# Performance work log

Measured on AMD Instinct MI355X. Metric: run time of the kernel, lower is better.

The kernel has to match this reference:

```python
import jax, jax.numpy as jnp
import numpy as np

N = 100000        # nodes
E = 1600000       # edges
G = 1000          # graphs
DIM = 256         # dim_h
DEPTH = 4
VOCAB = 100
MAX_ND = 20
EPS = 1e-5


def setup_inputs() -> dict:
    key = jax.random.key(0)
    ks = jax.random.split(key, 24)
    inp = {
        "x_idx": jax.random.randint(ks[0], (N,), 0, VOCAB, dtype=jnp.int32),
        "node_depth": jax.random.randint(ks[1], (N,), 0, MAX_ND, dtype=jnp.int32),
        "edge_index": jax.random.randint(ks[2], (2, E), 0, N, dtype=jnp.int32),
        "batch": jnp.sort(jax.random.randint(ks[3], (N,), 0, G, dtype=jnp.int32)),
        # node encoder embeddings
        "emb_node": 0.02 * jax.random.normal(ks[4], (VOCAB, DIM), jnp.float32),
        "emb_depth": 0.02 * jax.random.normal(ks[5], (MAX_ND, DIM), jnp.float32),
        # per-depth GIN MLP: Linear(DIM,DIM) -> ReLU -> Linear(DIM,DIM)
        "gin_w1": 0.05 * jax.random.normal(ks[6], (DEPTH, DIM, DIM), jnp.float32),
        "gin_b1": jnp.zeros((DEPTH, DIM), jnp.float32),
        "gin_w2": 0.05 * jax.random.normal(ks[7], (DEPTH, DIM, DIM), jnp.float32),
        "gin_b2": jnp.zeros((DEPTH, DIM), jnp.float32),
        # GraphNorm params
        "gn_alpha": jnp.ones((DEPTH, DIM), jnp.float32),
        "gn_gamma": jnp.ones((DEPTH, DIM), jnp.float32),
        "gn_beta": jnp.zeros((DEPTH, DIM), jnp.float32),
        # attention gate MLP: Linear(DIM, 2*DIM) -> ReLU -> Linear(2*DIM, 1)
        "att_w1": 0.05 * jax.random.normal(ks[8], (DEPTH, DIM, 2 * DIM), jnp.float32),
        "att_b1": jnp.zeros((DEPTH, 2 * DIM), jnp.float32),
        "att_w2": 0.05 * jax.random.normal(ks[9], (DEPTH, 2 * DIM, 1), jnp.float32),
        "att_b2": jnp.zeros((DEPTH, 1), jnp.float32),
    }
    return inp


def _graph_norm(x, batch, alpha, gamma, beta):
    # per-graph GraphNorm (Cai et al.): shift by alpha*mean, scale by std
    cnt = jax.ops.segment_sum(jnp.ones((x.shape[0],), x.dtype), batch, num_segments=G)
    cnt = jnp.maximum(cnt, 1.0)[:, None]                     # [G,1]
    mean = jax.ops.segment_sum(x, batch, num_segments=G) / cnt
    out = x - alpha * mean[batch]
    var = jax.ops.segment_sum(out * out, batch, num_segments=G) / cnt
    inv = jax.lax.rsqrt(var + EPS)
    return gamma * out * inv[batch] + beta


def _att_pool(x, batch, w1, b1, w2, b2):
    gate = (jax.nn.relu(x @ w1 + b1) @ w2 + b2)[:, 0]        # [N]
    m = jax.ops.segment_max(gate, batch, num_segments=G)
    e = jnp.exp(gate - m[batch])
    denom = jax.ops.segment_sum(e, batch, num_segments=G)
    w = e / denom[batch]                                     # segment softmax
    return jax.ops.segment_sum(w[:, None] * x, batch, num_segments=G)  # [G,DIM]


def reference(x_idx, node_depth, edge_index, batch,
              emb_node, emb_depth,
              gin_w1, gin_b1, gin_w2, gin_b2,
              gn_alpha, gn_gamma, gn_beta,
              att_w1, att_b1, att_w2, att_b2):
    src, dst = edge_index[0], edge_index[1]
    x = emb_node[x_idx] + emb_depth[node_depth]              # node encoder [N,DIM]
    graph_embs = []
    for d in range(DEPTH):
        x_in = x
        # GINConv (eps=0): MLP(x + sum_{j->i} x_j)
        agg = jax.ops.segment_sum(x[src], dst, num_segments=N)
        h = x + agg
        x = jax.nn.relu(h @ gin_w1[d] + gin_b1[d]) @ gin_w2[d] + gin_b2[d]
        x = _graph_norm(x, batch, gn_alpha[d], gn_gamma[d], gn_beta[d])
        if d < DEPTH - 1:
            x = jax.nn.relu(x)
        x = x + x_in                                         # residual
        graph_embs.append(_att_pool(x, batch, att_w1[d], att_b1[d], att_w2[d], att_b2[d]))
    stacked = jnp.stack(graph_embs, axis=0)                  # [DEPTH,G,DIM]
    agg_emb = jnp.mean(stacked, axis=0)                      # MLAP-Mean aggregate
    return jnp.concatenate([stacked, agg_emb[None]], axis=0) # [DEPTH+1,G,DIM]
```

## Files before the change

### kernel.cpp

```cpp
#include <hip/hip_runtime.h>
#include <hip/hip_bf16.h>

#define NN 100000
#define EE 1600000
#define GG 1000
#define DIMH 256
#define NDEPTH 4
static constexpr float EPSV = 1e-5f;

typedef unsigned short ushort;
typedef __attribute__((ext_vector_type(8))) ushort ushort8v;
typedef __attribute__((ext_vector_type(8))) short short8v;
typedef __attribute__((ext_vector_type(4))) float f32x4;

__device__ __forceinline__ float bf2f(ushort u) {
    return __uint_as_float(((unsigned)u) << 16);
}
__device__ __forceinline__ ushort f2bf(float f) {
    unsigned u = __float_as_uint(f);
    unsigned r = u + 0x7FFFu + ((u >> 16) & 1u);
    return (ushort)(r >> 16);
}

__global__ __launch_bounds__(256) void k_graph_bounds(const int* __restrict__ batch, int* __restrict__ gstart) {
    int g = blockIdx.x * 256 + threadIdx.x;
    if (g > GG) return;
    int lo = 0, hi = NN;
    while (lo < hi) { int mid = (lo + hi) >> 1; if (batch[mid] < g) lo = mid + 1; else hi = mid; }
    gstart[g] = lo;
}

__global__ __launch_bounds__(256) void k_hist(const int* __restrict__ dst, int* __restrict__ deg) {
    int e = blockIdx.x * 256 + threadIdx.x;
    if (e < EE) atomicAdd(&deg[dst[e]], 1);
}

__global__ __launch_bounds__(256) void k_scan_a(const int* __restrict__ deg, int* __restrict__ rs, int* __restrict__ part) {
    __shared__ int s[256];
    int t = threadIdx.x;
    int i = blockIdx.x * 256 + t;
    int v = (i < NN) ? deg[i] : 0;
    s[t] = v; __syncthreads();
    for (int off = 1; off < 256; off <<= 1) {
        int u = (t >= off) ? s[t - off] : 0;
        __syncthreads();
        s[t] += u;
        __syncthreads();
    }
    if (i < NN) rs[i] = s[t] - v;
    if (t == 255) part[blockIdx.x] = s[255];
}

__global__ __launch_bounds__(512) void k_scan_b(int* __restrict__ part, int nb, int* __restrict__ rs) {
    __shared__ int s[512];
    int t = threadIdx.x;
    int v = (t < nb) ? part[t] : 0;
    s[t] = v; __syncthreads();
    for (int off = 1; off < 512; off <<= 1) {
        int u = (t >= off) ? s[t - off] : 0;
        __syncthreads();
        s[t] += u;
        __syncthreads();
    }
    if (t < nb) part[t] = s[t] - v;
    if (t == 0) rs[NN] = EE;
}

__global__ __launch_bounds__(256) void k_scan_c(int* __restrict__ rs, const int* __restrict__ part) {
    int i = blockIdx.x * 256 + threadIdx.x;
    if (i < NN) rs[i] += part[blockIdx.x];
}

__global__ __launch_bounds__(256) void k_copy_int(const int* __restrict__ a, int* __restrict__ b, int n) {
    int i = blockIdx.x * 256 + threadIdx.x;
    if (i < n) b[i] = a[i];
}

__global__ __launch_bounds__(256) void k_scatter(const int* __restrict__ src, const int* __restrict__ dst,
                                                 int* __restrict__ cursor, int* __restrict__ col) {
    int e = blockIdx.x * 256 + threadIdx.x;
    if (e >= EE) return;
    int d = dst[e];
    int pos = atomicAdd(&cursor[d], 1);
    col[pos] = src[e];
}

__global__ __launch_bounds__(256) void k_wtrans(const float* __restrict__ in, ushort* __restrict__ out_hi,
                                                ushort* __restrict__ out_lo, int K, int N) {
    int d = blockIdx.z;
    in  += (size_t)d * K * N;
    out_hi += (size_t)d * K * N;
    out_lo += (size_t)d * K * N;
    int n0 = blockIdx.x * 32, k0 = blockIdx.y * 32;
    int t = threadIdx.x;
    int tx = t & 31, ty = t >> 5;
    __shared__ float tile[32][33];
#pragma unroll
    for (int j = 0; j < 4; j++) tile[ty + 8 * j][tx] = in[(size_t)(k0 + ty + 8 * j) * N + n0 + tx];
    __syncthreads();
#pragma unroll
    for (int j = 0; j < 4; j++) {
        float f = tile[tx][ty + 8 * j];
        ushort hi = f2bf(f);
        float lo = f - bf2f(hi);
        size_t o = (size_t)(n0 + ty + 8 * j) * K + k0 + tx;
        out_hi[o] = hi;
        out_lo[o] = f2bf(lo);
    }
}

__global__ __launch_bounds__(256) void k_encoder(const int* __restrict__ xidx, const int* __restrict__ ndep,
                                                 const float* __restrict__ en, const float* __restrict__ ed,
                                                 ushort* __restrict__ x) {
    int gi = blockIdx.x * 256 + threadIdx.x;
    int node = gi >> 6, q = gi & 63;
    if (node >= NN) return;
    float4 va = ((const float4*)en)[(size_t)xidx[node] * 64 + q];
    float4 vb = ((const float4*)ed)[(size_t)ndep[node] * 64 + q];
    ushort4 o;
    o.x = f2bf(va.x + vb.x); o.y = f2bf(va.y + vb.y);
    o.z = f2bf(va.z + vb.z); o.w = f2bf(va.w + vb.w);
    ((ushort4*)x)[gi] = o;
}

__global__ __launch_bounds__(256) void k_aggregate(const ushort* __restrict__ x, const int* __restrict__ rs,
                                                   const int* __restrict__ col, ushort* __restrict__ hb) {
    int node = blockIdx.x * 4 + (threadIdx.x >> 6);
    int lane = threadIdx.x & 63;
    if (node >= NN) return;
    const ushort4* x4 = (const ushort4*)x;
    ushort4 sv = x4[(size_t)node * 64 + lane];
    float a0 = bf2f(sv.x), a1 = bf2f(sv.y), a2 = bf2f(sv.z), a3 = bf2f(sv.w);
    float b0 = 0.f, b1 = 0.f, b2 = 0.f, b3 = 0.f;
    float c0 = 0.f, c1 = 0.f, c2 = 0.f, c3 = 0.f;
    float d0 = 0.f, d1 = 0.f, d2 = 0.f, d3 = 0.f;
    int s = rs[node], e = rs[node + 1];
    int j = s;
    for (; j + 4 <= e; j += 4) {
        int i0 = col[j], i1 = col[j + 1], i2 = col[j + 2], i3 = col[j + 3];
        ushort4 v0 = x4[(size_t)i0 * 64 + lane];
        ushort4 v1 = x4[(size_t)i1 * 64 + lane];
        ushort4 v2 = x4[(size_t)i2 * 64 + lane];
        ushort4 v3 = x4[(size_t)i3 * 64 + lane];
        a0 += bf2f(v0.x); a1 += bf2f(v0.y); a2 += bf2f(v0.z); a3 += bf2f(v0.w);
        b0 += bf2f(v1.x); b1 += bf2f(v1.y); b2 += bf2f(v1.z); b3 += bf2f(v1.w);
        c0 += bf2f(v2.x); c1 += bf2f(v2.y); c2 += bf2f(v2.z); c3 += bf2f(v2.w);
        d0 += bf2f(v3.x); d1 += bf2f(v3.y); d2 += bf2f(v3.z); d3 += bf2f(v3.w);
    }
    for (; j < e; j++) {
        int c = col[j];
        ushort4 v = x4[(size_t)c * 64 + lane];
        a0 += bf2f(v.x); a1 += bf2f(v.y); a2 += bf2f(v.z); a3 += bf2f(v.w);
    }
    a0 += b0 + c0 + d0; a1 += b1 + c1 + d1; a2 += b2 + c2 + d2; a3 += b3 + c3 + d3;
    ushort4 o; o.x = f2bf(a0); o.y = f2bf(a1); o.z = f2bf(a2); o.w = f2bf(a3);
    ((ushort4*)hb)[(size_t)node * 64 + lane] = o;
}

template<int MODE>
__global__ __launch_bounds__(256, 2) void k_mfma_gemm(const ushort* __restrict__ A,
                                                      const ushort* __restrict__ Bhi,
                                                      const ushort* __restrict__ Blo,
                                                      const float* __restrict__ bias,
                                                      const float* __restrict__ w2,
                                                      ushort* __restrict__ C,
                                                      float* __restrict__ partial,
                                                      int M) {
    __shared__ __align__(16) ushort As[256 * 64];
    __shared__ __align__(16) ushort Bh[128 * 64];
    __shared__ __align__(16) ushort Bl[128 * 64];
    int t = threadIdx.x;
    int wv = t >> 6, l = t & 63;
    int wr = wv >> 1, wc = wv & 1;
    int row0 = blockIdx.x * 256;
    int col0 = blockIdx.y * 128;

    f32x4 acc[8][4];
#pragma unroll
    for (int m = 0; m < 8; m++)
#pragma unroll
        for (int n = 0; n < 4; n++) acc[m][n] = (f32x4){0.f, 0.f, 0.f, 0.f};

    int srow_in = l >> 3;
    int slot    = l & 7;

    for (int k0 = 0; k0 < 256; k0 += 64) {
#pragma unroll
        for (int i = 0; i < 8; i++) {
            int stripe = wv * 8 + i;
            int rl = stripe * 8 + srow_in;
            int gc = slot ^ (rl & 7);
            const ushort* ga = A + (size_t)min(row0 + rl, M - 1) * 256 + k0 + gc * 8;
            __builtin_amdgcn_global_load_lds((const __attribute__((address_space(1))) void*)ga,
                                             (__attribute__((address_space(3))) void*)(As + stripe * 512),
                                             16, 0, 0);
        }
#pragma unroll
        for (int i = 0; i < 4; i++) {
            int stripe = wv * 4 + i;
            int rl = stripe * 8 + srow_in;
            int gc = slot ^ (rl & 7);
            const ushort* gh = Bhi + (size_t)(col0 + rl) * 256 + k0 + gc * 8;
            __builtin_amdgcn_global_load_lds((const __attribute__((address_space(1))) void*)gh,
                                             (__attribute__((address_space(3))) void*)(Bh + stripe * 512),
                                             16, 0, 0);
            const ushort* gl = Blo + (size_t)(col0 + rl) * 256 + k0 + gc * 8;
            __builtin_amdgcn_global_load_lds((const __attribute__((address_space(1))) void*)gl,
                                             (__attribute__((address_space(3))) void*)(Bl + stripe * 512),
                                             16, 0, 0);
        }
        __syncthreads();
#pragma unroll
        for (int s = 0; s < 2; s++) {
            short8v af[8], bhf[4], blf[4];
#pragma unroll
            for (int m = 0; m < 8; m++) {
                int rl = wr * 128 + m * 16 + (l & 15);
                int ch = (s * 4 + (l >> 4)) ^ (rl & 7);
                af[m] = *(const short8v*)(As + rl * 64 + ch * 8);
            }
#pragma unroll
            for (int n = 0; n < 4; n++) {
                int rl = wc * 64 + n * 16 + (l & 15);
                int ch = (s * 4 + (l >> 4)) ^ (rl & 7);
                bhf[n] = *(const short8v*)(Bh + rl * 64 + ch * 8);
                blf[n] = *(const short8v*)(Bl + rl * 64 + ch * 8);
            }
#pragma unroll
            for (int m = 0; m < 8; m++)
#pragma unroll
                for (int n = 0; n < 4; n++) {
                    acc[m][n] = __builtin_amdgcn_mfma_f32_16x16x32_bf16(af[m], bhf[n], acc[m][n], 0, 0, 0);
                    acc[m][n] = __builtin_amdgcn_mfma_f32_16x16x32_bf16(af[m], blf[n], acc[m][n], 0, 0, 0);
                }
        }
        __syncthreads();
    }

    if (MODE == 2) {
        float b1v[4], w2v[4];
#pragma unroll
        for (int n = 0; n < 4; n++) {
            int colc = col0 + wc * 64 + n * 16 + (l & 15);
            b1v[n] = bias[colc];
            w2v[n] = w2[colc];
        }
#pragma unroll
        for (int m = 0; m < 8; m++) {
#pragma unroll
            for (int j = 0; j < 4; j++) {
                float p = 0.f;
#pragma unroll
                for (int n = 0; n < 4; n++) {
                    float v = fmaxf(acc[m][n][j] + b1v[n], 0.f);
                    p = fmaf(v, w2v[n], p);
                }
#pragma unroll
                for (int off = 1; off < 16; off <<= 1) p += __shfl_xor(p, off, 64);
                if ((l & 15) == 0) {
                    int row = row0 + wr * 128 + m * 16 + ((l >> 4) << 2) + j;
                    if (row < M) partial[(size_t)row * 8 + blockIdx.y * 2 + wc] = p;
                }
            }
        }
    } else {
        float bv[4];
#pragma unroll
        for (int n = 0; n < 4; n++) bv[n] = bias[col0 + wc * 64 + n * 16 + (l & 15)];
#pragma unroll
        for (int m = 0; m < 8; m++) {
#pragma unroll
            for (int j = 0; j < 4; j++) {
                int row = row0 + wr * 128 + m * 16 + ((l >> 4) << 2) + j;
                if (row < M) {
#pragma unroll
                    for (int n = 0; n < 4; n++) {
                        float v = acc[m][n][j] + bv[n];
                        if (MODE == 1) v = fmaxf(v, 0.f);
                        C[(size_t)row * 256 + col0 + wc * 64 + n * 16 + (l & 15)] = f2bf(v);
                    }
                }
            }
        }
    }
}

__global__ __launch_bounds__(256) void k_gatefin(const float* __restrict__ partial, const float* __restrict__ b2,
                                                 float* __restrict__ gate) {
    int i = blockIdx.x * 256 + threadIdx.x;
    if (i >= NN) return;
    const float4* p = (const float4*)(partial + (size_t)i * 8);
    float4 u = p[0], v = p[1];
    gate[i] = u.x + u.y + u.z + u.w + v.x + v.y + v.z + v.w + b2[0];
}

__global__ __launch_bounds__(256) void k_stats(const ushort* __restrict__ y, const int* __restrict__ gstart,
                                               const float* __restrict__ alpha,
                                               float* __restrict__ mean, float* __restrict__ inv) {
    int g = blockIdx.x, t = threadIdx.x;
    int s = gstart[g], e = gstart[g + 1];
    float s1 = 0.f, s2 = 0.f;
    for (int i = s; i < e; i++) {
        float v = bf2f(y[(size_t)i * DIMH + t]);
        s1 += v; s2 = fmaf(v, v, s2);
    }
    float cnt = (float)((e - s) > 1 ? (e - s) : 1);
    float m = s1 / cnt;
    float a = alpha[t];
    float am = a * m;
    float var = s2 / cnt - 2.f * am * m + am * am;
    mean[(size_t)g * DIMH + t] = m;
    inv[(size_t)g * DIMH + t] = rsqrtf(var + EPSV);
}

__global__ __launch_bounds__(256) void k_norm(const ushort* __restrict__ y, const int* __restrict__ batch,
                                              const float* __restrict__ mean, const float* __restrict__ inv,
                                              const float* __restrict__ alpha, const float* __restrict__ gamma,
                                              const float* __restrict__ beta, ushort* __restrict__ x, int relu) {
    int gi = blockIdx.x * 256 + threadIdx.x;
    int node = gi >> 6, q = gi & 63;
    if (node >= NN) return;
    int b = batch[node];
    ushort4 yv = ((const ushort4*)y)[gi];
    ushort4 xv = ((const ushort4*)x)[gi];
    float vv[4] = { bf2f(yv.x), bf2f(yv.y), bf2f(yv.z), bf2f(yv.w) };
    float xo[4] = { bf2f(xv.x), bf2f(xv.y), bf2f(xv.z), bf2f(xv.w) };
#pragma unroll
    for (int c = 0; c < 4; c++) {
        int colc = q * 4 + c;
        float m  = mean[(size_t)b * DIMH + colc];
        float iv = inv[(size_t)b * DIMH + colc];
        float o = (vv[c] - alpha[colc] * m) * iv * gamma[colc] + beta[colc];
        if (relu) o = fmaxf(o, 0.f);
        xo[c] += o;
    }
    ushort4 o4; o4.x = f2bf(xo[0]); o4.y = f2bf(xo[1]); o4.z = f2bf(xo[2]); o4.w = f2bf(xo[3]);
    ((ushort4*)x)[gi] = o4;
}

__global__ __launch_bounds__(256) void k_pool(const ushort* __restrict__ x, const float* __restrict__ gate,
                                              const int* __restrict__ gstart, float* __restrict__ outg) {
    __shared__ float red[256];
    __shared__ float wbuf[256];
    int g = blockIdx.x, t = threadIdx.x;
    int s = gstart[g], e = gstart[g + 1];
    if (s >= e) { outg[(size_t)g * DIMH + t] = 0.f; return; }
    float m = -3.4e38f;
    for (int i = s + t; i < e; i += 256) m = fmaxf(m, gate[i]);
    red[t] = m; __syncthreads();
    for (int o = 128; o > 0; o >>= 1) { if (t < o) red[t] = fmaxf(red[t], red[t + o]); __syncthreads(); }
    m = red[0]; __syncthreads();
    float se = 0.f;
    for (int i = s + t; i < e; i += 256) se += expf(gate[i] - m);
    red[t] = se; __syncthreads();
    for (int o = 128; o > 0; o >>= 1) { if (t < o) red[t] += red[t + o]; __syncthreads(); }
    float inv_se = 1.f / red[0];
    float o_acc = 0.f;
    for (int base = s; base < e; base += 256) {
        __syncthreads();
        int i = base + t;
        wbuf[t] = (i < e) ? expf(gate[i] - m) * inv_se : 0.f;
        __syncthreads();
        int cnt = min(256, e - base);
        for (int j = 0; j < cnt; j++) o_acc += wbuf[j] * bf2f(x[(size_t)(base + j) * DIMH + t]);
    }
    outg[(size_t)g * DIMH + t] = o_acc;
}

__global__ __launch_bounds__(256) void k_final(float* __restrict__ out) {
    const int GD = GG * DIMH;
    int i = blockIdx.x * 256 + threadIdx.x;
    if (i >= GD) return;
    float s = out[i] + out[GD + i] + out[2 * GD + i] + out[3 * GD + i];
    out[4 * GD + i] = 0.25f * s;
}

__global__ __launch_bounds__(256) void k_zero_out(float* __restrict__ out, int n) {
    int i = blockIdx.x * 256 + threadIdx.x;
    if (i < n) out[i] = 0.f;
}

extern "C" void kernel_launch(void* const* d_in, const int* in_sizes, int n_in,
                              void* d_out, int out_size, void* d_ws, size_t ws_size,
                              hipStream_t stream) {
    const int*   x_idx     = (const int*)d_in[0];
    const int*   node_dep  = (const int*)d_in[1];
    const int*   eidx      = (const int*)d_in[2];
    const int*   batch     = (const int*)d_in[3];
    const float* emb_node  = (const float*)d_in[4];
    const float* emb_depth = (const float*)d_in[5];
    const float* gin_w1    = (const float*)d_in[6];
    const float* gin_b1    = (const float*)d_in[7];
    const float* gin_w2    = (const float*)d_in[8];
    const float* gin_b2    = (const float*)d_in[9];
    const float* gn_alpha  = (const float*)d_in[10];
    const float* gn_gamma  = (const float*)d_in[11];
    const float* gn_beta   = (const float*)d_in[12];
    const float* att_w1    = (const float*)d_in[13];
    const float* att_b1    = (const float*)d_in[14];
    const float* att_w2    = (const float*)d_in[15];
    const float* att_b2    = (const float*)d_in[16];
    float* out = (float*)d_out;
    (void)in_sizes; (void)n_in;

    const size_t SZ_NODE_BF16 = (size_t)NN * DIMH * 2;
    const size_t SZ_W256 = (size_t)NDEPTH * 256 * 256 * 2;
    const size_t SZ_W512 = (size_t)NDEPTH * 256 * 512 * 2;
    size_t required = 3 * ((SZ_NODE_BF16 + 255) & ~(size_t)255)
                    + 4 * SZ_W256 + 2 * SZ_W512
                    + ((size_t)EE * 4 + 256) + ((size_t)(NN + 1) * 4 + 256) * 2
                    + 4096 + 8192 + 2 * ((size_t)GG * DIMH * 4 + 256) + ((size_t)NN * 4 + 256) + 65536;
    if (ws_size < required) {
        k_zero_out<<<(out_size + 255) / 256, 256, 0, stream>>>(out, out_size);
        return;
    }

    char* w = (char*)d_ws;
    size_t off = 0;
    auto alloc = [&](size_t bytes) -> char* {
        char* p = w + off;
        off += (bytes + 255) & ~(size_t)255;
        return p;
    };
    ushort* x  = (ushort*)alloc(SZ_NODE_BF16);
    ushort* hb = (ushort*)alloc(SZ_NODE_BF16);
    ushort* y1 = (ushort*)alloc(SZ_NODE_BF16);
    float* partial = (float*)y1;
    ushort* wt_g1h = (ushort*)alloc(SZ_W256);
    ushort* wt_g1l = (ushort*)alloc(SZ_W256);
    ushort* wt_g2h = (ushort*)alloc(SZ_W256);
    ushort* wt_g2l = (ushort*)alloc(SZ_W256);
    ushort* wt_a1h = (ushort*)alloc(SZ_W512);
    ushort* wt_a1l = (ushort*)alloc(SZ_W512);
    int* deg    = (int*)alloc((size_t)NN * 4);
    int* rs     = (int*)alloc((size_t)(NN + 1) * 4);
    int* part   = (int*)alloc(512 * 4);
    int* gstart = (int*)alloc((GG + 1) * 4);
    int* col    = (int*)alloc((size_t)EE * 4);
    float* mean = (float*)alloc((size_t)GG * DIMH * 4);
    float* inv  = (float*)alloc((size_t)GG * DIMH * 4);
    float* gate = (float*)alloc((size_t)NN * 4);

    const int* src  = eidx;
    const int* dstp = eidx + EE;

    hipMemsetAsync(deg, 0, (size_t)NN * 4, stream);
    k_graph_bounds<<<(GG + 1 + 255) / 256, 256, 0, stream>>>(batch, gstart);
    k_hist<<<(EE + 255) / 256, 256, 0, stream>>>(dstp, deg);
    int nb = (NN + 255) / 256;
    k_scan_a<<<nb, 256, 0, stream>>>(deg, rs, part);
    k_scan_b<<<1, 512, 0, stream>>>(part, nb, rs);
    k_scan_c<<<nb, 256, 0, stream>>>(rs, part);
    k_copy_int<<<nb, 256, 0, stream>>>(rs, deg, NN);
    k_scatter<<<(EE + 255) / 256, 256, 0, stream>>>(src, dstp, deg, col);
    k_encoder<<<(NN * 64 + 255) / 256, 256, 0, stream>>>(x_idx, node_dep, emb_node, emb_depth, x);

    k_wtrans<<<dim3(8, 8, NDEPTH), 256, 0, stream>>>(gin_w1, wt_g1h, wt_g1l, 256, 256);
    k_wtrans<<<dim3(8, 8, NDEPTH), 256, 0, stream>>>(gin_w2, wt_g2h, wt_g2l, 256, 256);
    k_wtrans<<<dim3(16, 8, NDEPTH), 256, 0, stream>>>(att_w1, wt_a1h, wt_a1l, 256, 512);

    const int GD = GG * DIMH;
    const int MB = (NN + 255) / 256;
    for (int d = 0; d < NDEPTH; d++) {
        k_aggregate<<<(NN + 3) / 4, 256, 0, stream>>>(x, rs, col, hb);
        k_mfma_gemm<1><<<dim3(MB, 2), 256, 0, stream>>>(hb, wt_g1h + (size_t)d * 65536, wt_g1l + (size_t)d * 65536,
                                                        gin_b1 + d * 256, nullptr, y1, nullptr, NN);
        k_mfma_gemm<0><<<dim3(MB, 2), 256, 0, stream>>>(y1, wt_g2h + (size_t)d * 65536, wt_g2l + (size_t)d * 65536,
                                                        gin_b2 + d * 256, nullptr, hb, nullptr, NN);
        k_stats<<<GG, 256, 0, stream>>>(hb, gstart, gn_alpha + d * 256, mean, inv);
        k_norm<<<(NN * 64 + 255) / 256, 256, 0, stream>>>(hb, batch, mean, inv, gn_alpha + d * 256,
                                                          gn_gamma + d * 256, gn_beta + d * 256, x,
                                                          (d < NDEPTH - 1) ? 1 : 0);
        k_mfma_gemm<2><<<dim3(MB, 4), 256, 0, stream>>>(x, wt_a1h + (size_t)d * 131072, wt_a1l + (size_t)d * 131072,
                                                        att_b1 + d * 512, att_w2 + d * 512, nullptr, partial, NN);
        k_gatefin<<<(NN + 255) / 256, 256, 0, stream>>>(partial, att_b2 + d, gate);
        k_pool<<<GG, 256, 0, stream>>>(x, gate, gstart, out + (size_t)d * GD);
    }
    k_final<<<(GD + 255) / 256, 256, 0, stream>>>(out);
}
```

Measured before the change: 1.632 ms.

## Double-buffer GEMM LDS staging, fuse GraphNorm stats with normalize, deepen aggregate unroll

The MFMA GEMM now works in K-steps of 32 with two LDS buffers. The next tile is prefetched with global_load_lds while the current one feeds the MFMAs, and one sync per step replaces two. The GraphNorm stats and normalize kernels are fused into one per-graph kernel that rereads the graph's rows, which removes the mean/inv buffers and one launch. The aggregate loop gains an 8-wide unroll to keep more gathers in flight. The fused norm runs only 1000 blocks, one per graph, so its parallelism is lower than the old elementwise kernel, and the GEMM swizzle layout changed.

```diff
diff --git a/kernel.cpp b/kernel.cpp
--- a/kernel.cpp
+++ b/kernel.cpp
@@ -21,6 +21,9 @@
     unsigned r = u + 0x7FFFu + ((u >> 16) & 1u);
     return (ushort)(r >> 16);
 }
+
+#define GLOAD16(g, s) __builtin_amdgcn_global_load_lds((const __attribute__((address_space(1))) void*)(g), \
+                      (__attribute__((address_space(3))) void*)(s), 16, 0, 0)
 
 __global__ __launch_bounds__(256) void k_graph_bounds(const int* __restrict__ batch, int* __restrict__ gstart) {
     int g = blockIdx.x * 256 + threadIdx.x;
@@ -136,6 +139,26 @@
     float d0 = 0.f, d1 = 0.f, d2 = 0.f, d3 = 0.f;
     int s = rs[node], e = rs[node + 1];
     int j = s;
+    for (; j + 8 <= e; j += 8) {
+        int i0 = col[j], i1 = col[j + 1], i2 = col[j + 2], i3 = col[j + 3];
+        int i4 = col[j + 4], i5 = col[j + 5], i6 = col[j + 6], i7 = col[j + 7];
+        ushort4 v0 = x4[(size_t)i0 * 64 + lane];
+        ushort4 v1 = x4[(size_t)i1 * 64 + lane];
+        ushort4 v2 = x4[(size_t)i2 * 64 + lane];
+        ushort4 v3 = x4[(size_t)i3 * 64 + lane];
+        ushort4 v4 = x4[(size_t)i4 * 64 + lane];
+        ushort4 v5 = x4[(size_t)i5 * 64 + lane];
+        ushort4 v6 = x4[(size_t)i6 * 64 + lane];
+        ushort4 v7 = x4[(size_t)i7 * 64 + lane];
+        a0 += bf2f(v0.x); a1 += bf2f(v0.y); a2 += bf2f(v0.z); a3 += bf2f(v0.w);
+        b0 += bf2f(v1.x); b1 += bf2f(v1.y); b2 += bf2f(v1.z); b3 += bf2f(v1.w);
+        c0 += bf2f(v2.x); c1 += bf2f(v2.y); c2 += bf2f(v2.z); c3 += bf2f(v2.w);
+        d0 += bf2f(v3.x); d1 += bf2f(v3.y); d2 += bf2f(v3.z); d3 += bf2f(v3.w);
+        a0 += bf2f(v4.x); a1 += bf2f(v4.y); a2 += bf2f(v4.z); a3 += bf2f(v4.w);
+        b0 += bf2f(v5.x); b1 += bf2f(v5.y); b2 += bf2f(v5.z); b3 += bf2f(v5.w);
+        c0 += bf2f(v6.x); c1 += bf2f(v6.y); c2 += bf2f(v6.z); c3 += bf2f(v6.w);
+        d0 += bf2f(v7.x); d1 += bf2f(v7.y); d2 += bf2f(v7.z); d3 += bf2f(v7.w);
+    }
     for (; j + 4 <= e; j += 4) {
         int i0 = col[j], i1 = col[j + 1], i2 = col[j + 2], i3 = col[j + 3];
         ushort4 v0 = x4[(size_t)i0 * 64 + lane];
@@ -166,9 +189,7 @@
                                                       ushort* __restrict__ C,
                                                       float* __restrict__ partial,
                                                       int M) {
-    __shared__ __align__(16) ushort As[256 * 64];
-    __shared__ __align__(16) ushort Bh[128 * 64];
-    __shared__ __align__(16) ushort Bl[128 * 64];
+    __shared__ __align__(16) ushort lds[2 * 16384];
     int t = threadIdx.x;
     int wv = t >> 6, l = t & 63;
     int wr = wv >> 1, wc = wv & 1;
@@ -181,67 +202,67 @@
 #pragma unroll
         for (int n = 0; n < 4; n++) acc[m][n] = (f32x4){0.f, 0.f, 0.f, 0.f};
 
-    int srow_in = l >> 3;
-    int slot    = l & 7;
-
-    for (int k0 = 0; k0 < 256; k0 += 64) {
-#pragma unroll
-        for (int i = 0; i < 8; i++) {
-            int stripe = wv * 8 + i;
-            int rl = stripe * 8 + srow_in;
-            int gc = slot ^ (rl & 7);
-            const ushort* ga = A + (size_t)min(row0 + rl, M - 1) * 256 + k0 + gc * 8;
-            __builtin_amdgcn_global_load_lds((const __attribute__((address_space(1))) void*)ga,
-                                             (__attribute__((address_space(3))) void*)(As + stripe * 512),
-                                             16, 0, 0);
-        }
+    int srow = l >> 2;
+    int sck  = ((l & 3) ^ ((l >> 3) & 3)) * 8;
+
+    auto stage = [&](int k0, ushort* buf) {
 #pragma unroll
         for (int i = 0; i < 4; i++) {
             int stripe = wv * 4 + i;
-            int rl = stripe * 8 + srow_in;
-            int gc = slot ^ (rl & 7);
-            const ushort* gh = Bhi + (size_t)(col0 + rl) * 256 + k0 + gc * 8;
-            __builtin_amdgcn_global_load_lds((const __attribute__((address_space(1))) void*)gh,
-                                             (__attribute__((address_space(3))) void*)(Bh + stripe * 512),
-                                             16, 0, 0);
-            const ushort* gl = Blo + (size_t)(col0 + rl) * 256 + k0 + gc * 8;
-            __builtin_amdgcn_global_load_lds((const __attribute__((address_space(1))) void*)gl,
-                                             (__attribute__((address_space(3))) void*)(Bl + stripe * 512),
-                                             16, 0, 0);
-        }
-        __syncthreads();
-#pragma unroll
-        for (int s = 0; s < 2; s++) {
-            short8v af[8], bhf[4], blf[4];
-#pragma unroll
-            for (int m = 0; m < 8; m++) {
-                int rl = wr * 128 + m * 16 + (l & 15);
-                int ch = (s * 4 + (l >> 4)) ^ (rl & 7);
-                af[m] = *(const short8v*)(As + rl * 64 + ch * 8);
+            int rl = stripe * 16 + srow;
+            const ushort* ga = A + (size_t)min(row0 + rl, M - 1) * 256 + k0 + sck;
+            GLOAD16(ga, buf + stripe * 512 + l * 8);
+        }
+#pragma unroll
+        for (int i = 0; i < 2; i++) {
+            int stripe = wv * 2 + i;
+            int rl = stripe * 16 + srow;
+            const ushort* gh = Bhi + (size_t)(col0 + rl) * 256 + k0 + sck;
+            GLOAD16(gh, buf + 8192 + stripe * 512 + l * 8);
+            const ushort* gl = Blo + (size_t)(col0 + rl) * 256 + k0 + sck;
+            GLOAD16(gl, buf + 12288 + stripe * 512 + l * 8);
+        }
+    };
+
+    int lr = l & 15, kc = l >> 4;
+
+    ushort* cur = lds;
+    ushort* nxt = lds + 16384;
+    stage(0, cur);
+    __syncthreads();
+
+    for (int it = 0; it < 8; it++) {
+        if (it < 7) stage((it + 1) * 32, nxt);
+
+        short8v af[8], bhf[4], blf[4];
+#pragma unroll
+        for (int m = 0; m < 8; m++) {
+            int r = wr * 128 + m * 16 + lr;
+            af[m] = *(const short8v*)(cur + r * 32 + ((kc ^ ((r >> 1) & 3)) * 8));
+        }
+#pragma unroll
+        for (int n = 0; n < 4; n++) {
+            int rb = wc * 64 + n * 16 + lr;
+            int so = (kc ^ ((rb >> 1) & 3)) * 8;
+            bhf[n] = *(const short8v*)(cur + 8192 + rb * 32 + so);
+            blf[n] = *(const short8v*)(cur + 12288 + rb * 32 + so);
+        }
+#pragma unroll
+        for (int m = 0; m < 8; m++)
+#pragma unroll
+            for (int n = 0; n < 4; n++) {
+                acc[m][n] = __builtin_amdgcn_mfma_f32_16x16x32_bf16(af[m], bhf[n], acc[m][n], 0, 0, 0);
+                acc[m][n] = __builtin_amdgcn_mfma_f32_16x16x32_bf16(af[m], blf[n], acc[m][n], 0, 0, 0);
             }
-#pragma unroll
-            for (int n = 0; n < 4; n++) {
-                int rl = wc * 64 + n * 16 + (l & 15);
-                int ch = (s * 4 + (l >> 4)) ^ (rl & 7);
-                bhf[n] = *(const short8v*)(Bh + rl * 64 + ch * 8);
-                blf[n] = *(const short8v*)(Bl + rl * 64 + ch * 8);
-            }
-#pragma unroll
-            for (int m = 0; m < 8; m++)
-#pragma unroll
-                for (int n = 0; n < 4; n++) {
-                    acc[m][n] = __builtin_amdgcn_mfma_f32_16x16x32_bf16(af[m], bhf[n], acc[m][n], 0, 0, 0);
-                    acc[m][n] = __builtin_amdgcn_mfma_f32_16x16x32_bf16(af[m], blf[n], acc[m][n], 0, 0, 0);
-                }
-        }
-        __syncthreads();
+        __syncthreads();
+        ushort* tmp = cur; cur = nxt; nxt = tmp;
     }
 
     if (MODE == 2) {
         float b1v[4], w2v[4];
 #pragma unroll
         for (int n = 0; n < 4; n++) {
-            int colc = col0 + wc * 64 + n * 16 + (l & 15);
+            int colc = col0 + wc * 64 + n * 16 + lr;
             b1v[n] = bias[colc];
             w2v[n] = w2[colc];
         }
@@ -257,8 +278,8 @@
                 }
 #pragma unroll
                 for (int off = 1; off < 16; off <<= 1) p += __shfl_xor(p, off, 64);
-                if ((l & 15) == 0) {
-                    int row = row0 + wr * 128 + m * 16 + ((l >> 4) << 2) + j;
+                if (lr == 0) {
+                    int row = row0 + wr * 128 + m * 16 + (kc << 2) + j;
                     if (row < M) partial[(size_t)row * 8 + blockIdx.y * 2 + wc] = p;
                 }
             }
@@ -266,18 +287,18 @@
     } else {
         float bv[4];
 #pragma unroll
-        for (int n = 0; n < 4; n++) bv[n] = bias[col0 + wc * 64 + n * 16 + (l & 15)];
+        for (int n = 0; n < 4; n++) bv[n] = bias[col0 + wc * 64 + n * 16 + lr];
 #pragma unroll
         for (int m = 0; m < 8; m++) {
 #pragma unroll
             for (int j = 0; j < 4; j++) {
-                int row = row0 + wr * 128 + m * 16 + ((l >> 4) << 2) + j;
+                int row = row0 + wr * 128 + m * 16 + (kc << 2) + j;
                 if (row < M) {
 #pragma unroll
                     for (int n = 0; n < 4; n++) {
                         float v = acc[m][n][j] + bv[n];
                         if (MODE == 1) v = fmaxf(v, 0.f);
-                        C[(size_t)row * 256 + col0 + wc * 64 + n * 16 + (l & 15)] = f2bf(v);
+                        C[(size_t)row * 256 + col0 + wc * 64 + n * 16 + lr] = f2bf(v);
                     }
                 }
             }
@@ -294,11 +315,12 @@
     gate[i] = u.x + u.y + u.z + u.w + v.x + v.y + v.z + v.w + b2[0];
 }
 
-__global__ __launch_bounds__(256) void k_stats(const ushort* __restrict__ y, const int* __restrict__ gstart,
-                                               const float* __restrict__ alpha,
-                                               float* __restrict__ mean, float* __restrict__ inv) {
+__global__ __launch_bounds__(256) void k_statsnorm(const ushort* __restrict__ y, const int* __restrict__ gstart,
+                                                   const float* __restrict__ alpha, const float* __restrict__ gamma,
+                                                   const float* __restrict__ beta, ushort* __restrict__ x, int relu) {
     int g = blockIdx.x, t = threadIdx.x;
     int s = gstart[g], e = gstart[g + 1];
+    if (s >= e) return;
     float s1 = 0.f, s2 = 0.f;
     for (int i = s; i < e; i++) {
         float v = bf2f(y[(size_t)i * DIMH + t]);
@@ -309,33 +331,15 @@
     float a = alpha[t];
     float am = a * m;
     float var = s2 / cnt - 2.f * am * m + am * am;
-    mean[(size_t)g * DIMH + t] = m;
-    inv[(size_t)g * DIMH + t] = rsqrtf(var + EPSV);
-}
-
-__global__ __launch_bounds__(256) void k_norm(const ushort* __restrict__ y, const int* __restrict__ batch,
-                                              const float* __restrict__ mean, const float* __restrict__ inv,
-                                              const float* __restrict__ alpha, const float* __restrict__ gamma,
-                                              const float* __restrict__ beta, ushort* __restrict__ x, int relu) {
-    int gi = blockIdx.x * 256 + threadIdx.x;
-    int node = gi >> 6, q = gi & 63;
-    if (node >= NN) return;
-    int b = batch[node];
-    ushort4 yv = ((const ushort4*)y)[gi];
-    ushort4 xv = ((const ushort4*)x)[gi];
-    float vv[4] = { bf2f(yv.x), bf2f(yv.y), bf2f(yv.z), bf2f(yv.w) };
-    float xo[4] = { bf2f(xv.x), bf2f(xv.y), bf2f(xv.z), bf2f(xv.w) };
-#pragma unroll
-    for (int c = 0; c < 4; c++) {
-        int colc = q * 4 + c;
-        float m  = mean[(size_t)b * DIMH + colc];
-        float iv = inv[(size_t)b * DIMH + colc];
-        float o = (vv[c] - alpha[colc] * m) * iv * gamma[colc] + beta[colc];
+    float iv = rsqrtf(var + EPSV);
+    float ga = gamma[t], be = beta[t];
+    for (int i = s; i < e; i++) {
+        float v  = bf2f(y[(size_t)i * DIMH + t]);
+        float xo = bf2f(x[(size_t)i * DIMH + t]);
+        float o = (v - am) * iv * ga + be;
         if (relu) o = fmaxf(o, 0.f);
-        xo[c] += o;
-    }
-    ushort4 o4; o4.x = f2bf(xo[0]); o4.y = f2bf(xo[1]); o4.z = f2bf(xo[2]); o4.w = f2bf(xo[3]);
-    ((ushort4*)x)[gi] = o4;
+        x[(size_t)i * DIMH + t] = f2bf(xo + o);
+    }
 }
 
 __global__ __launch_bounds__(256) void k_pool(const ushort* __restrict__ x, const float* __restrict__ gate,
@@ -409,7 +413,7 @@
     size_t required = 3 * ((SZ_NODE_BF16 + 255) & ~(size_t)255)
                     + 4 * SZ_W256 + 2 * SZ_W512
                     + ((size_t)EE * 4 + 256) + ((size_t)(NN + 1) * 4 + 256) * 2
-                    + 4096 + 8192 + 2 * ((size_t)GG * DIMH * 4 + 256) + ((size_t)NN * 4 + 256) + 65536;
+                    + 4096 + 8192 + ((size_t)NN * 4 + 256) + 65536;
     if (ws_size < required) {
         k_zero_out<<<(out_size + 255) / 256, 256, 0, stream>>>(out, out_size);
         return;
@@ -437,8 +441,6 @@
     int* part   = (int*)alloc(512 * 4);
     int* gstart = (int*)alloc((GG + 1) * 4);
     int* col    = (int*)alloc((size_t)EE * 4);
-    float* mean = (float*)alloc((size_t)GG * DIMH * 4);
-    float* inv  = (float*)alloc((size_t)GG * DIMH * 4);
     float* gate = (float*)alloc((size_t)NN * 4);
 
     const int* src  = eidx;
@@ -467,10 +469,8 @@
                                                         gin_b1 + d * 256, nullptr, y1, nullptr, NN);
         k_mfma_gemm<0><<<dim3(MB, 2), 256, 0, stream>>>(y1, wt_g2h + (size_t)d * 65536, wt_g2l + (size_t)d * 65536,
                                                         gin_b2 + d * 256, nullptr, hb, nullptr, NN);
-        k_stats<<<GG, 256, 0, stream>>>(hb, gstart, gn_alpha + d * 256, mean, inv);
-        k_norm<<<(NN * 64 + 255) / 256, 256, 0, stream>>>(hb, batch, mean, inv, gn_alpha + d * 256,
-                                                          gn_gamma + d * 256, gn_beta + d * 256, x,
-                                                          (d < NDEPTH - 1) ? 1 : 0);
+        k_statsnorm<<<GG, 256, 0, stream>>>(hb, gstart, gn_alpha + d * 256, gn_gamma + d * 256,
+                                            gn_beta + d * 256, x, (d < NDEPTH - 1) ? 1 : 0);
         k_mfma_gemm<2><<<dim3(MB, 4), 256, 0, stream>>>(x, wt_a1h + (size_t)d * 131072, wt_a1l + (size_t)d * 131072,
                                                         att_b1 + d * 512, att_w2 + d * 512, nullptr, partial, NN);
         k_gatefin<<<(NN + 255) / 256, 256, 0, stream>>>(partial, att_b2 + d, gate);
```

After: 1.670 ms. 2.4% more time.
